# Performance work log

Hardware: AMD Instinct MI355X
Metric: run time of the kernel (lower is better)

The kernel has to match this reference:

```python
import jax, jax.numpy as jnp
import numpy as np

N_NODES = 50000
N_EDGES = 800000
HID = 128
N_PROC = 3  # num_layers - 1 processor iterations (shared weights)


def _mlp(x, w1, b1, w2, b2, w3, b3):
    h = jax.nn.relu(x @ w1 + b1)
    h = jax.nn.relu(h @ w2 + b2)
    return h @ w3 + b3


def setup_inputs() -> dict:
    key = jax.random.key(0)
    ks = jax.random.split(key, 32)

    def p(k, shape):
        fan_in = shape[0]
        return (jax.random.normal(k, shape, dtype=jnp.float32) / np.float32(np.sqrt(fan_in)))

    inp = {
        "X_curr": jax.random.normal(ks[0], (N_NODES, 6), dtype=jnp.float32),
        "y_prev": jax.random.normal(ks[1], (N_NODES,), dtype=jnp.float32),
        "edge": jax.random.randint(ks[2], (2, N_EDGES), 0, N_NODES, dtype=jnp.int32),
        "mode": 0,
        # EdgeModel net: Linear(9,H) ReLU Linear(H,H) ReLU Linear(H,3)
        "ew1": p(ks[3], (9, HID)), "eb1": jnp.zeros((HID,), jnp.float32),
        "ew2": p(ks[4], (HID, HID)), "eb2": jnp.zeros((HID,), jnp.float32),
        "ew3": p(ks[5], (HID, 3)), "eb3": jnp.zeros((3,), jnp.float32),
        # NodeModel net: Linear(5,H) ReLU Linear(H,H) ReLU Linear(H,1)
        "nw1": p(ks[6], (5, HID)), "nb1": jnp.zeros((HID,), jnp.float32),
        "nw2": p(ks[7], (HID, HID)), "nb2": jnp.zeros((HID,), jnp.float32),
        "nw3": p(ks[8], (HID, 1)), "nb3": jnp.zeros((1,), jnp.float32),
        # decoder: Linear(5,H) ReLU Linear(H,H) ReLU Linear(H,H) ReLU Linear(H,1)
        "dw1": p(ks[9], (5, HID)), "db1": jnp.zeros((HID,), jnp.float32),
        "dw2": p(ks[10], (HID, HID)), "db2": jnp.zeros((HID,), jnp.float32),
        "dw3": p(ks[11], (HID, HID)), "db3": jnp.zeros((HID,), jnp.float32),
        "dw4": p(ks[12], (HID, 1)), "db4": jnp.zeros((1,), jnp.float32),
    }
    return inp


def reference(X_curr, y_prev,
              ew1, eb1, ew2, eb2, ew3, eb3,
              nw1, nb1, nw2, nb2, nw3, nb3,
              dw1, db1, dw2, db2, dw3, db3, dw4, db4,
              edge, mode):
    n = X_curr.shape[0]
    src_idx, dst_idx = edge[0], edge[1]
    # x_in = cat(X_curr[:, [0,1,2,4]], y_prev)  -> [N, 5]
    x = jnp.concatenate([X_curr[:, jnp.array([0, 1, 2, 4])], y_prev[:, None]], axis=-1)

    # _compute_edge_attr: grad_r = (f_dest - f_src) * disp_r
    xs, xd = x[src_idx], x[dst_idx]
    disp = xd[:, :3] - xs[:, :3]
    edge_attr = (xd[:, 4] - xs[:, 4])[:, None] * disp  # [E, 3]

    # degree for scatter-mean (nodes with no incoming edges aggregate to 0)
    deg = jax.ops.segment_sum(jnp.ones((edge.shape[1],), x.dtype), dst_idx, num_segments=n)
    inv_deg = jnp.where(deg > 0, 1.0 / jnp.maximum(deg, 1.0), 0.0)

    for _ in range(N_PROC):
        # EdgeModel
        xs, xd = x[src_idx], x[dst_idx]
        disp = xd[:, :3] - xs[:, :3]
        norm_r = jnp.linalg.norm(disp, axis=-1, keepdims=True)
        net_in = jnp.concatenate([disp, norm_r, edge_attr, xs[:, 4:5], xd[:, 4:5]], axis=-1)  # [E, 9]
        edge_attr = edge_attr + _mlp(net_in, ew1, eb1, ew2, eb2, ew3, eb3)
        # NodeModel: message = edge_attr, aggr='mean' at target (edge[1])
        aggr = jax.ops.segment_sum(edge_attr, dst_idx, num_segments=n) * inv_deg[:, None]  # [N, 3]
        node_in = jnp.concatenate([x[:, 3:5], aggr], axis=-1)  # [N, 5]
        delta = _mlp(node_in, nw1, nb1, nw2, nb2, nw3, nb3)[:, 0]
        x = x.at[:, 4].add(delta)

    # decoder
    h = jax.nn.relu(x @ dw1 + db1)
    h = jax.nn.relu(h @ dw2 + db2)
    h = jax.nn.relu(h @ dw3 + db3)
    x_out = h @ dw4 + db4  # [N, 1]
    return y_prev + x_out[:, 0]
```

## Files before the change

kernel.cpp:

```cpp
#include <hip/hip_runtime.h>

typedef float f32x4 __attribute__((ext_vector_type(4)));
typedef __bf16 bf16x8 __attribute__((ext_vector_type(8)));
typedef __bf16 bf16x4 __attribute__((ext_vector_type(4)));

#define WB_W1E 0
#define WB_W2E 4096
#define WB_W3E 20480
#define WB_W1N 22528
#define WB_W2N 26624
#define WB_W3N 43008
#define WB_W1D 45056
#define WB_W2D 49152
#define WB_W3D 65536
#define WB_W4D 81920
#define WB_TOTAL 83968

#define BKT_SHIFT 6
#define BKT_SZ 64

__global__ void k_prep(const float* __restrict__ ew1, const float* __restrict__ eb1,
                       const float* __restrict__ ew2, const float* __restrict__ ew3,
                       const float* __restrict__ nw1, const float* __restrict__ nb1,
                       const float* __restrict__ nw2, const float* __restrict__ nw3,
                       const float* __restrict__ dw1, const float* __restrict__ db1,
                       const float* __restrict__ dw2, const float* __restrict__ dw3,
                       const float* __restrict__ dw4, __bf16* __restrict__ wb) {
  int gid = blockIdx.x * 256 + threadIdx.x;
  if (gid >= WB_TOTAL) return;
  const float* srcs[10] = {ew1, ew2, ew3, nw1, nw2, nw3, dw1, dw2, dw3, dw4};
  const float* brow[10] = {eb1, 0, 0, nb1, 0, 0, db1, 0, 0, 0};
  const int Ks[10] = {9, 128, 128, 5, 128, 128, 5, 128, 128, 128};
  const int Ns[10] = {128, 128, 3, 128, 128, 1, 128, 128, 128, 1};
  const int CTs[10] = {8, 8, 1, 8, 8, 1, 8, 8, 8, 1};
  const int cum[11] = {0, 4096, 20480, 22528, 26624, 43008, 45056, 49152, 65536, 81920, 83968};
  int seg = 0;
  while (gid >= cum[seg + 1]) seg++;
  int li = gid - cum[seg];
  int j = li & 7;
  int lane = (li >> 3) & 63;
  int fi = li >> 9;
  int CT = CTs[seg];
  int ct = fi % CT;
  int kt = fi / CT;
  int k = kt * 32 + ((lane >> 4) << 3) + j;
  int n = ct * 16 + (lane & 15);
  int kl;
  if (seg == 0) {
    if (k < 4) kl = k;
    else if (k >= 8 && k < 13) kl = k - 4;
    else kl = (k == 13) ? -2 : -1;
  } else if (seg == 3 || seg == 6) {
    if (k < 5) kl = k;
    else kl = (k == 5) ? -2 : -1;
  } else {
    kl = (k < Ks[seg]) ? k : -1;
  }
  float v = 0.f;
  if (n < Ns[seg]) {
    if (kl >= 0) v = srcs[seg][kl * Ns[seg] + n];
    else if (kl == -2 && brow[seg]) v = brow[seg][n];
  }
  wb[gid] = (__bf16)v;
}

__global__ void k_zero(const float* __restrict__ y_prev, float* __restrict__ x4,
                       int* __restrict__ cnt, int n) {
  int i = blockIdx.x * 256 + threadIdx.x;
  if (i < n) {
    x4[i] = y_prev[i];
    cnt[i] = 0;
  }
}

__global__ void k_count(const int* __restrict__ dstp, int* __restrict__ cnt, int E) {
  int e = blockIdx.x * 256 + threadIdx.x;
  if (e < E) atomicAdd(cnt + dstp[e], 1);
}

__global__ void k_scan_block(const int* __restrict__ cnt, int* __restrict__ rp,
                             float* __restrict__ invdeg, int* __restrict__ bsum, int n) {
  __shared__ int sd[256];
  int t = threadIdx.x;
  int i = blockIdx.x * 256 + t;
  int c = (i < n) ? cnt[i] : 0;
  if (i < n) invdeg[i] = c > 0 ? 1.0f / (float)c : 0.f;
  sd[t] = c;
  __syncthreads();
#pragma unroll
  for (int off = 1; off < 256; off <<= 1) {
    int v = sd[t];
    int u = (t >= off) ? sd[t - off] : 0;
    __syncthreads();
    sd[t] = v + u;
    __syncthreads();
  }
  if (i < n) rp[i] = sd[t] - c;
  if (t == 255) bsum[blockIdx.x] = sd[255];
}

__global__ void k_scan_top(int* __restrict__ bsum, int nb) {
  __shared__ int sd[1024];
  int t = threadIdx.x;
  int c = (t < nb) ? bsum[t] : 0;
  sd[t] = c;
  __syncthreads();
#pragma unroll
  for (int off = 1; off < 1024; off <<= 1) {
    int v = sd[t];
    int u = (t >= off) ? sd[t - off] : 0;
    __syncthreads();
    sd[t] = v + u;
    __syncthreads();
  }
  if (t < nb) bsum[t] = sd[t] - c;
}

__global__ void k_scan_add(int* __restrict__ rp, const int* __restrict__ bsum, int n, int E) {
  int i = blockIdx.x * 256 + threadIdx.x;
  if (i < n) rp[i] += bsum[blockIdx.x];
  if (i == 0) rp[n] = E;
}

__global__ void k_initcur(const int* __restrict__ rp, int* __restrict__ cur, int nbkt, int n) {
  int b = blockIdx.x * 256 + threadIdx.x;
  if (b < nbkt) {
    int d = b << BKT_SHIFT;
    if (d > n) d = n;
    cur[b] = rp[d];
  }
}

__global__ __launch_bounds__(256) void k_bin(const int* __restrict__ dstp, int* __restrict__ cur,
                                             int* __restrict__ eix, int nbkt, int E) {
  __shared__ int hist[1024];
  __shared__ int base[1024];
  int tid = threadIdx.x;
  for (int t = tid; t < nbkt; t += 256) hist[t] = 0;
  __syncthreads();
  int e0 = blockIdx.x * 8192;
  int b[32], lr[32];
#pragma unroll
  for (int j = 0; j < 32; j++) {
    int e = e0 + j * 256 + tid;
    if (e < E) {
      b[j] = dstp[e] >> BKT_SHIFT;
      lr[j] = atomicAdd(&hist[b[j]], 1);
    } else {
      b[j] = -1;
      lr[j] = 0;
    }
  }
  __syncthreads();
  for (int t = tid; t < nbkt; t += 256) {
    int c = hist[t];
    base[t] = c ? atomicAdd(&cur[t], c) : 0;
  }
  __syncthreads();
#pragma unroll
  for (int j = 0; j < 32; j++)
    if (b[j] >= 0) eix[base[b[j]] + lr[j]] = e0 + j * 256 + tid;
}

__global__ __launch_bounds__(256) void k_build(const int* __restrict__ srcO,
                                               const int* __restrict__ dstO,
                                               const float* __restrict__ Xc,
                                               const float* __restrict__ yp,
                                               const int* __restrict__ rp, const int* eix,
                                               int* __restrict__ srcS, int* dstS,
                                               float* __restrict__ peS, float* __restrict__ eaS,
                                               int n) {
  __shared__ int rpl[BKT_SZ + 1];
  __shared__ int cnt[BKT_SZ];
  int tid = threadIdx.x;
  int d0 = blockIdx.x << BKT_SHIFT;
  if (tid <= BKT_SZ) {
    int d = d0 + tid;
    if (d > n) d = n;
    rpl[tid] = rp[d];
  }
  if (tid < BKT_SZ) cnt[tid] = 0;
  __syncthreads();
  int dlim = n - d0;
  if (dlim > BKT_SZ) dlim = BKT_SZ;
  int gstart = rpl[0], gend = rpl[dlim];
  int ei[16];
#pragma unroll
  for (int k = 0; k < 16; k++) {
    int p = gstart + k * 256 + tid;
    ei[k] = (p < gend) ? eix[p] : -1;
  }
  __syncthreads();
#pragma unroll
  for (int k = 0; k < 16; k++) {
    int e = ei[k];
    if (e < 0) continue;
    int s = srcO[e], d = dstO[e];
    float dx = Xc[d * 6 + 0] - Xc[s * 6 + 0];
    float dy = Xc[d * 6 + 1] - Xc[s * 6 + 1];
    float dz = Xc[d * 6 + 2] - Xc[s * 6 + 2];
    float nr = sqrtf(dx * dx + dy * dy + dz * dz);
    float w = yp[d] - yp[s];
    int r = atomicAdd(&cnt[d - d0], 1);
    int q = rpl[d - d0] + r;
    srcS[q] = s;
    dstS[q] = d;
    f32x4 pv = {dx, dy, dz, nr};
    *(f32x4*)(peS + 4 * q) = pv;
    f32x4 av = {w * dx, w * dy, w * dz, 0.f};
    *(f32x4*)(eaS + 4 * q) = av;
  }
}

__global__ void k_gather(const float* __restrict__ eaS, const int* __restrict__ rp,
                         const float* __restrict__ invdeg, float* __restrict__ aggr, int n) {
  int i = blockIdx.x * 256 + threadIdx.x;
  if (i >= n) return;
  int s = rp[i];
  int e = rp[i + 1];
  f32x4 acc = {0.f, 0.f, 0.f, 0.f};
#pragma unroll 2
  for (int p = s; p < e; p++) {
    f32x4 v = *(const f32x4*)(eaS + 4 * p);
    acc[0] += v[0];
    acc[1] += v[1];
    acc[2] += v[2];
  }
  float iv = invdeg[i];
  f32x4 o = {acc[0] * iv, acc[1] * iv, acc[2] * iv, 0.f};
  *(f32x4*)(aggr + 4 * i) = o;
}

__device__ __forceinline__ int aoff(int row, int b) { return (row * 256 + b) ^ ((row & 7) << 4); }

__device__ __forceinline__ void wg_sync() {
  asm volatile("s_waitcnt lgkmcnt(0)" ::: "memory");
  __builtin_amdgcn_s_barrier();
}

__device__ __forceinline__ bf16x4 relu_pack(f32x4 a) {
  bf16x4 p;
#pragma unroll
  for (int r = 0; r < 4; r++) {
    float v = a[r];
    p[r] = (__bf16)(v > 0.f ? v : 0.f);
  }
  return p;
}

__global__ __attribute__((amdgpu_flat_work_group_size(256, 256), amdgpu_waves_per_eu(3, 4))) void
k_edge(const float* __restrict__ x4, const float* __restrict__ pe, float* __restrict__ ea,
       const int* __restrict__ src, const int* __restrict__ dstp,
       const __bf16* __restrict__ W1f, const __bf16* __restrict__ W2f,
       const __bf16* __restrict__ W3f, const float* __restrict__ b2,
       const float* __restrict__ b3, int ntiles, int E) {
  __shared__ char Ab[16384];
  __shared__ char Bb[16384];
  const int tid = threadIdx.x;
  const int l = tid & 63, w = tid >> 6;
  const int col = l & 15, krow = l >> 4;
  const int rl = w * 16 + (l >> 2), chunk = l & 3;

  bf16x8 w1r[2], w2r[4][2], w3r[4];
#pragma unroll
  for (int t = 0; t < 2; t++) w1r[t] = *(const bf16x8*)(W1f + ((2 * w + t) << 9) + l * 8);
#pragma unroll
  for (int kt = 0; kt < 4; kt++)
#pragma unroll
    for (int t = 0; t < 2; t++)
      w2r[kt][t] = *(const bf16x8*)(W2f + ((kt * 8 + 2 * w + t) << 9) + l * 8);
#pragma unroll
  for (int kt = 0; kt < 4; kt++) w3r[kt] = *(const bf16x8*)(W3f + (kt << 9) + l * 8);
  f32x4 b2c[2];
#pragma unroll
  for (int t = 0; t < 2; t++) b2c[t] = *(const f32x4*)(b2 + (2 * w + t) * 16 + krow * 4);
  f32x4 b3i = {0.f, 0.f, 0.f, 0.f};
  if (krow == 0) {
    b3i[0] = b3[0];
    b3i[1] = b3[1];
    b3i[2] = b3[2];
  }

  int tile = blockIdx.x;
  if (tile >= ntiles) return;

  int e0 = tile * 64 + rl;
  int ec = e0 < E ? e0 : E - 1;
  int cs = src[ec], cd = dstp[ec];
  f32x4 cld = {0.f, 0.f, 0.f, 0.f};
  if (chunk < 2) cld = *(const f32x4*)(((chunk == 1) ? ea : pe) + 4 * ec);
  float cxs = 0.f, cxd = 0.f;
  if (chunk == 1) {
    cxs = x4[cs];
    cxd = x4[cd];
  }

  for (;;) {
    bf16x8 v;
#pragma unroll
    for (int q = 0; q < 8; q++) v[q] = (__bf16)0.f;
    if (chunk == 0) {
      v[0] = (__bf16)cld[0];
      v[1] = (__bf16)cld[1];
      v[2] = (__bf16)cld[2];
      v[3] = (__bf16)cld[3];
    } else if (chunk == 1) {
      v[0] = (__bf16)cld[0];
      v[1] = (__bf16)cld[1];
      v[2] = (__bf16)cld[2];
      v[3] = (__bf16)cxs;
      v[4] = (__bf16)cxd;
      v[5] = (__bf16)1.0f;
    }
    *(bf16x8*)(Ab + aoff(rl, chunk * 16)) = v;

    int nt = tile + (int)gridDim.x;
    bool hn = nt < ntiles;
    int tc = hn ? nt : tile;
    int en = tc * 64 + rl;
    if (en >= E) en = E - 1;
    int ns = src[en], nd = dstp[en];

    wg_sync();

    f32x4 h[4][2];
#pragma unroll
    for (int c = 0; c < 4; c++)
#pragma unroll
      for (int t = 0; t < 2; t++) {
        f32x4 z = {0.f, 0.f, 0.f, 0.f};
        h[c][t] = z;
      }
    bf16x8 bb[4];
#pragma unroll
    for (int c = 0; c < 4; c++) bb[c] = *(const bf16x8*)(Ab + aoff(c * 16 + col, krow * 16));
#pragma unroll
    for (int c = 0; c < 4; c++)
#pragma unroll
      for (int t = 0; t < 2; t++)
        h[c][t] = __builtin_amdgcn_mfma_f32_16x16x32_bf16(w1r[t], bb[c], h[c][t], 0, 0, 0);
#pragma unroll
    for (int c = 0; c < 4; c++)
#pragma unroll
      for (int t = 0; t < 2; t++)
        *(bf16x4*)(Bb + aoff(c * 16 + col, (2 * w + t) * 32 + krow * 8)) = relu_pack(h[c][t]);

    wg_sync();

    f32x4 nld = {0.f, 0.f, 0.f, 0.f};
    if (chunk < 2) nld = *(const f32x4*)(((chunk == 1) ? ea : pe) + 4 * en);
    float nxs = 0.f, nxd = 0.f;
    if (chunk == 1) {
      nxs = x4[ns];
      nxd = x4[nd];
    }

#pragma unroll
    for (int c = 0; c < 4; c++)
#pragma unroll
      for (int t = 0; t < 2; t++) h[c][t] = b2c[t];
#pragma unroll
    for (int kt = 0; kt < 4; kt++) {
#pragma unroll
      for (int c = 0; c < 4; c++)
        bb[c] = *(const bf16x8*)(Bb + aoff(c * 16 + col, kt * 64 + krow * 16));
#pragma unroll
      for (int c = 0; c < 4; c++)
#pragma unroll
        for (int t = 0; t < 2; t++)
          h[c][t] = __builtin_amdgcn_mfma_f32_16x16x32_bf16(w2r[kt][t], bb[c], h[c][t], 0, 0, 0);
    }
#pragma unroll
    for (int c = 0; c < 4; c++)
#pragma unroll
      for (int t = 0; t < 2; t++)
        *(bf16x4*)(Ab + aoff(c * 16 + col, (2 * w + t) * 32 + krow * 8)) = relu_pack(h[c][t]);

    wg_sync();

    f32x4 o = b3i;
#pragma unroll
    for (int kt = 0; kt < 4; kt++) {
      bf16x8 bq = *(const bf16x8*)(Ab + aoff(w * 16 + col, kt * 64 + krow * 16));
      o = __builtin_amdgcn_mfma_f32_16x16x32_bf16(w3r[kt], bq, o, 0, 0, 0);
    }

    if (krow == 0) {
      int e3 = tile * 64 + w * 16 + col;
      if (e3 < E) {
        f32x4 oe = *(const f32x4*)(ea + 4 * e3);
        f32x4 nv;
        nv[0] = oe[0] + o[0];
        nv[1] = oe[1] + o[1];
        nv[2] = oe[2] + o[2];
        nv[3] = 0.f;
        *(f32x4*)(ea + 4 * e3) = nv;
      }
    }

    if (!hn) break;
    tile = nt;
    cld = nld;
    cxs = nxs;
    cxd = nxd;
  }
}

__global__ __attribute__((amdgpu_flat_work_group_size(256, 256), amdgpu_waves_per_eu(3, 4))) void
k_node(float* __restrict__ x4, const float* __restrict__ Xc, const float* __restrict__ aggr,
       const __bf16* __restrict__ W1f, const __bf16* __restrict__ W2f,
       const __bf16* __restrict__ W3f, const float* __restrict__ b2,
       const float* __restrict__ b3, int n) {
  __shared__ char Ab[16384];
  __shared__ char Bb[16384];
  const int tid = threadIdx.x;
  const int l = tid & 63, w = tid >> 6;
  const int col = l & 15, krow = l >> 4;
  const int rl = w * 16 + (l >> 2), chunk = l & 3;

  bf16x8 w1r[2], w2r[4][2], w3r[4];
#pragma unroll
  for (int t = 0; t < 2; t++) w1r[t] = *(const bf16x8*)(W1f + ((2 * w + t) << 9) + l * 8);
#pragma unroll
  for (int kt = 0; kt < 4; kt++)
#pragma unroll
    for (int t = 0; t < 2; t++)
      w2r[kt][t] = *(const bf16x8*)(W2f + ((kt * 8 + 2 * w + t) << 9) + l * 8);
#pragma unroll
  for (int kt = 0; kt < 4; kt++) w3r[kt] = *(const bf16x8*)(W3f + (kt << 9) + l * 8);
  f32x4 b2c[2];
#pragma unroll
  for (int t = 0; t < 2; t++) b2c[t] = *(const f32x4*)(b2 + (2 * w + t) * 16 + krow * 4);
  float b3s = b3[0];

  int tile = blockIdx.x;
  int i0 = tile * 64 + rl;
  bool vi = i0 < n;
  int i = vi ? i0 : (n - 1);

  bf16x8 v;
#pragma unroll
  for (int q = 0; q < 8; q++) v[q] = (__bf16)0.f;
  if (chunk == 0) {
    float x3 = Xc[i * 6 + 4];
    float xv = x4[i];
    f32x4 ag = *(const f32x4*)(aggr + 4 * i);
    v[0] = (__bf16)x3;
    v[1] = (__bf16)xv;
    v[2] = (__bf16)ag[0];
    v[3] = (__bf16)ag[1];
    v[4] = (__bf16)ag[2];
    v[5] = (__bf16)1.0f;
  }
  *(bf16x8*)(Ab + aoff(rl, chunk * 16)) = v;

  wg_sync();

  f32x4 h[4][2];
#pragma unroll
  for (int c = 0; c < 4; c++)
#pragma unroll
    for (int t = 0; t < 2; t++) {
      f32x4 z = {0.f, 0.f, 0.f, 0.f};
      h[c][t] = z;
    }
  bf16x8 bb[4];
#pragma unroll
  for (int c = 0; c < 4; c++) bb[c] = *(const bf16x8*)(Ab + aoff(c * 16 + col, krow * 16));
#pragma unroll
  for (int c = 0; c < 4; c++)
#pragma unroll
    for (int t = 0; t < 2; t++)
      h[c][t] = __builtin_amdgcn_mfma_f32_16x16x32_bf16(w1r[t], bb[c], h[c][t], 0, 0, 0);
#pragma unroll
  for (int c = 0; c < 4; c++)
#pragma unroll
    for (int t = 0; t < 2; t++)
      *(bf16x4*)(Bb + aoff(c * 16 + col, (2 * w + t) * 32 + krow * 8)) = relu_pack(h[c][t]);

  wg_sync();

#pragma unroll
  for (int c = 0; c < 4; c++)
#pragma unroll
    for (int t = 0; t < 2; t++) h[c][t] = b2c[t];
#pragma unroll
  for (int kt = 0; kt < 4; kt++) {
#pragma unroll
    for (int c = 0; c < 4; c++)
      bb[c] = *(const bf16x8*)(Bb + aoff(c * 16 + col, kt * 64 + krow * 16));
#pragma unroll
    for (int c = 0; c < 4; c++)
#pragma unroll
      for (int t = 0; t < 2; t++)
        h[c][t] = __builtin_amdgcn_mfma_f32_16x16x32_bf16(w2r[kt][t], bb[c], h[c][t], 0, 0, 0);
  }
#pragma unroll
  for (int c = 0; c < 4; c++)
#pragma unroll
    for (int t = 0; t < 2; t++)
      *(bf16x4*)(Ab + aoff(c * 16 + col, (2 * w + t) * 32 + krow * 8)) = relu_pack(h[c][t]);

  wg_sync();

  f32x4 o = {0.f, 0.f, 0.f, 0.f};
  if (krow == 0) o[0] = b3s;
#pragma unroll
  for (int kt = 0; kt < 4; kt++) {
    bf16x8 bq = *(const bf16x8*)(Ab + aoff(w * 16 + col, kt * 64 + krow * 16));
    o = __builtin_amdgcn_mfma_f32_16x16x32_bf16(w3r[kt], bq, o, 0, 0, 0);
  }

  if (krow == 0) {
    int i3 = tile * 64 + w * 16 + col;
    if (i3 < n) x4[i3] = x4[i3] + o[0];
  }
}

__global__ __attribute__((amdgpu_flat_work_group_size(256, 256), amdgpu_waves_per_eu(2, 4))) void
k_dec(const float* __restrict__ x4, const float* __restrict__ Xc, const float* __restrict__ y_prev,
      const __bf16* __restrict__ W1f, const __bf16* __restrict__ W2f,
      const __bf16* __restrict__ W3f, const __bf16* __restrict__ W4f,
      const float* __restrict__ b2, const float* __restrict__ b3, const float* __restrict__ b4,
      float* __restrict__ out, int n) {
  __shared__ char Ab[16384];
  __shared__ char Bb[16384];
  const int tid = threadIdx.x;
  const int l = tid & 63, w = tid >> 6;
  const int col = l & 15, krow = l >> 4;
  const int rl = w * 16 + (l >> 2), chunk = l & 3;

  bf16x8 w1r[2], w2r[4][2], w3r[4][2], w4r[4];
#pragma unroll
  for (int t = 0; t < 2; t++) w1r[t] = *(const bf16x8*)(W1f + ((2 * w + t) << 9) + l * 8);
#pragma unroll
  for (int kt = 0; kt < 4; kt++)
#pragma unroll
    for (int t = 0; t < 2; t++) {
      w2r[kt][t] = *(const bf16x8*)(W2f + ((kt * 8 + 2 * w + t) << 9) + l * 8);
      w3r[kt][t] = *(const bf16x8*)(W3f + ((kt * 8 + 2 * w + t) << 9) + l * 8);
    }
#pragma unroll
  for (int kt = 0; kt < 4; kt++) w4r[kt] = *(const bf16x8*)(W4f + (kt << 9) + l * 8);
  f32x4 b2c[2], b3c[2];
#pragma unroll
  for (int t = 0; t < 2; t++) {
    b2c[t] = *(const f32x4*)(b2 + (2 * w + t) * 16 + krow * 4);
    b3c[t] = *(const f32x4*)(b3 + (2 * w + t) * 16 + krow * 4);
  }
  float b4s = b4[0];

  int tile = blockIdx.x;
  int i0 = tile * 64 + rl;
  bool vi = i0 < n;
  int i = vi ? i0 : (n - 1);

  bf16x8 v;
#pragma unroll
  for (int q = 0; q < 8; q++) v[q] = (__bf16)0.f;
  if (chunk == 0) {
    v[0] = (__bf16)Xc[i * 6 + 0];
    v[1] = (__bf16)Xc[i * 6 + 1];
    v[2] = (__bf16)Xc[i * 6 + 2];
    v[3] = (__bf16)Xc[i * 6 + 4];
    v[4] = (__bf16)x4[i];
    v[5] = (__bf16)1.0f;
  }
  *(bf16x8*)(Ab + aoff(rl, chunk * 16)) = v;

  wg_sync();

  f32x4 h[4][2];
  bf16x8 bb[4];
#pragma unroll
  for (int c = 0; c < 4; c++)
#pragma unroll
    for (int t = 0; t < 2; t++) {
      f32x4 z = {0.f, 0.f, 0.f, 0.f};
      h[c][t] = z;
    }
#pragma unroll
  for (int c = 0; c < 4; c++) bb[c] = *(const bf16x8*)(Ab + aoff(c * 16 + col, krow * 16));
#pragma unroll
  for (int c = 0; c < 4; c++)
#pragma unroll
    for (int t = 0; t < 2; t++)
      h[c][t] = __builtin_amdgcn_mfma_f32_16x16x32_bf16(w1r[t], bb[c], h[c][t], 0, 0, 0);
#pragma unroll
  for (int c = 0; c < 4; c++)
#pragma unroll
    for (int t = 0; t < 2; t++)
      *(bf16x4*)(Bb + aoff(c * 16 + col, (2 * w + t) * 32 + krow * 8)) = relu_pack(h[c][t]);

  wg_sync();

#pragma unroll
  for (int c = 0; c < 4; c++)
#pragma unroll
    for (int t = 0; t < 2; t++) h[c][t] = b2c[t];
#pragma unroll
  for (int kt = 0; kt < 4; kt++) {
#pragma unroll
    for (int c = 0; c < 4; c++)
      bb[c] = *(const bf16x8*)(Bb + aoff(c * 16 + col, kt * 64 + krow * 16));
#pragma unroll
    for (int c = 0; c < 4; c++)
#pragma unroll
      for (int t = 0; t < 2; t++)
        h[c][t] = __builtin_amdgcn_mfma_f32_16x16x32_bf16(w2r[kt][t], bb[c], h[c][t], 0, 0, 0);
  }
#pragma unroll
  for (int c = 0; c < 4; c++)
#pragma unroll
    for (int t = 0; t < 2; t++)
      *(bf16x4*)(Ab + aoff(c * 16 + col, (2 * w + t) * 32 + krow * 8)) = relu_pack(h[c][t]);

  wg_sync();

#pragma unroll
  for (int c = 0; c < 4; c++)
#pragma unroll
    for (int t = 0; t < 2; t++) h[c][t] = b3c[t];
#pragma unroll
  for (int kt = 0; kt < 4; kt++) {
#pragma unroll
    for (int c = 0; c < 4; c++)
      bb[c] = *(const bf16x8*)(Ab + aoff(c * 16 + col, kt * 64 + krow * 16));
#pragma unroll
    for (int c = 0; c < 4; c++)
#pragma unroll
      for (int t = 0; t < 2; t++)
        h[c][t] = __builtin_amdgcn_mfma_f32_16x16x32_bf16(w3r[kt][t], bb[c], h[c][t], 0, 0, 0);
  }
#pragma unroll
  for (int c = 0; c < 4; c++)
#pragma unroll
    for (int t = 0; t < 2; t++)
      *(bf16x4*)(Bb + aoff(c * 16 + col, (2 * w + t) * 32 + krow * 8)) = relu_pack(h[c][t]);

  wg_sync();

  f32x4 o = {0.f, 0.f, 0.f, 0.f};
  if (krow == 0) o[0] = b4s;
#pragma unroll
  for (int kt = 0; kt < 4; kt++) {
    bf16x8 bq = *(const bf16x8*)(Bb + aoff(w * 16 + col, kt * 64 + krow * 16));
    o = __builtin_amdgcn_mfma_f32_16x16x32_bf16(w4r[kt], bq, o, 0, 0, 0);
  }

  if (krow == 0) {
    int i3 = tile * 64 + w * 16 + col;
    if (i3 < n) out[i3] = y_prev[i3] + o[0];
  }
}

extern "C" void kernel_launch(void* const* d_in, const int* in_sizes, int n_in, void* d_out,
                              int out_size, void* d_ws, size_t ws_size, hipStream_t stream) {
  const float* Xc = (const float*)d_in[0];
  const float* y_prev = (const float*)d_in[1];
  const int* edge = (const int*)d_in[2];
  const float* ew1 = (const float*)d_in[4];
  const float* eb1 = (const float*)d_in[5];
  const float* ew2 = (const float*)d_in[6];
  const float* eb2 = (const float*)d_in[7];
  const float* ew3 = (const float*)d_in[8];
  const float* eb3 = (const float*)d_in[9];
  const float* nw1 = (const float*)d_in[10];
  const float* nb1 = (const float*)d_in[11];
  const float* nw2 = (const float*)d_in[12];
  const float* nb2 = (const float*)d_in[13];
  const float* nw3 = (const float*)d_in[14];
  const float* nb3 = (const float*)d_in[15];
  const float* dw1 = (const float*)d_in[16];
  const float* db1 = (const float*)d_in[17];
  const float* dw2 = (const float*)d_in[18];
  const float* db2 = (const float*)d_in[19];
  const float* dw3 = (const float*)d_in[20];
  const float* db3 = (const float*)d_in[21];
  const float* dw4 = (const float*)d_in[22];
  const float* db4 = (const float*)d_in[23];

  int n = in_sizes[0] / 6;
  int E = in_sizes[2] / 2;
  const int* srcp = edge;
  const int* dstp = edge + E;

  __bf16* wb = (__bf16*)d_ws;
  float* fbase = (float*)((char*)d_ws + (size_t)WB_TOTAL * 2);
  size_t na = ((size_t)n + 3) & ~(size_t)3;
  float* x4 = fbase;
  float* invdeg = fbase + na;
  float* aggr = fbase + 2 * na;
  int* cnt = (int*)(fbase + 6 * na);
  int* rp = cnt + na;
  int* bsum = rp + na + 8;
  int* srcS = bsum + 1024;
  int* dstS = srcS + E;
  float* peS = (float*)(dstS + E);
  float* eaS = peS + 4 * (size_t)E;

  size_t need = (size_t)WB_TOTAL * 2 + (8 * na + 8 + 1024 + 10 * (size_t)E) * 4;
  if (ws_size < need) return;

  dim3 B(256);
  int nblk = (n + 255) / 256;
  int nbkt = (n + BKT_SZ - 1) / BKT_SZ;
  k_prep<<<dim3((WB_TOTAL + 255) / 256), B, 0, stream>>>(ew1, eb1, ew2, ew3, nw1, nb1, nw2, nw3,
                                                         dw1, db1, dw2, dw3, dw4, wb);
  k_zero<<<dim3(nblk), B, 0, stream>>>(y_prev, x4, cnt, n);
  k_count<<<dim3((E + 255) / 256), B, 0, stream>>>(dstp, cnt, E);
  k_scan_block<<<dim3(nblk), B, 0, stream>>>(cnt, rp, invdeg, bsum, n);
  k_scan_top<<<dim3(1), dim3(1024), 0, stream>>>(bsum, nblk);
  k_scan_add<<<dim3(nblk), B, 0, stream>>>(rp, bsum, n, E);
  k_initcur<<<dim3((nbkt + 255) / 256), B, 0, stream>>>(rp, bsum, nbkt, n);
  k_bin<<<dim3((E + 8191) / 8192), B, 0, stream>>>(dstp, bsum, dstS, nbkt, E);
  k_build<<<dim3(nbkt), B, 0, stream>>>(srcp, dstp, Xc, y_prev, rp, dstS, srcS, dstS, peS, eaS, n);

  int etiles = (E + 63) / 64;
  int vtiles = (n + 63) / 64;
  int egrid = etiles < 768 ? etiles : 768;
  for (int it = 0; it < 3; it++) {
    k_edge<<<dim3(egrid), B, 0, stream>>>(x4, peS, eaS, srcS, dstS, wb + WB_W1E, wb + WB_W2E,
                                          wb + WB_W3E, eb2, eb3, etiles, E);
    k_gather<<<dim3((n + 255) / 256), B, 0, stream>>>(eaS, rp, invdeg, aggr, n);
    k_node<<<dim3(vtiles), B, 0, stream>>>(x4, Xc, aggr, wb + WB_W1N, wb + WB_W2N, wb + WB_W3N,
                                           nb2, nb3, n);
  }
  k_dec<<<dim3(vtiles), B, 0, stream>>>(x4, Xc, y_prev, wb + WB_W1D, wb + WB_W2D, wb + WB_W3D,
                                        wb + WB_W4D, db2, db3, db4, (float*)d_out, n);
}
```

Baseline: 303.1 us.

## Fuse segment-mean gather into node kernel and fold cursor init into scan

Removes the separate k_gather kernel. Each node row's four lanes now sum its CSR-sorted edge attributes with a strided loop and shuffle reduction inside k_node, which drops the aggr buffer round-trip and one launch per iteration. The bucket cursor initialisation moves into k_scan_add, removing the k_initcur launch. The edge kernel's waves_per_eu hint is widened and its persistent grid cap raised from 768 to 2048 blocks, trading register budget for more resident waves.

```diff
diff --git a/kernel.cpp b/kernel.cpp
--- a/kernel.cpp
+++ b/kernel.cpp
@@ -116,19 +116,15 @@
   if (t < nb) bsum[t] = sd[t] - c;
 }
 
-__global__ void k_scan_add(int* __restrict__ rp, const int* __restrict__ bsum, int n, int E) {
+__global__ void k_scan_add(int* __restrict__ rp, const int* __restrict__ bsum,
+                           int* __restrict__ cur, int n, int E) {
   int i = blockIdx.x * 256 + threadIdx.x;
-  if (i < n) rp[i] += bsum[blockIdx.x];
+  if (i < n) {
+    int v = rp[i] + bsum[blockIdx.x];
+    rp[i] = v;
+    if ((i & (BKT_SZ - 1)) == 0) cur[i >> BKT_SHIFT] = v;
+  }
   if (i == 0) rp[n] = E;
-}
-
-__global__ void k_initcur(const int* __restrict__ rp, int* __restrict__ cur, int nbkt, int n) {
-  int b = blockIdx.x * 256 + threadIdx.x;
-  if (b < nbkt) {
-    int d = b << BKT_SHIFT;
-    if (d > n) d = n;
-    cur[b] = rp[d];
-  }
 }
 
 __global__ __launch_bounds__(256) void k_bin(const int* __restrict__ dstp, int* __restrict__ cur,
@@ -212,25 +208,6 @@
   }
 }
 
-__global__ void k_gather(const float* __restrict__ eaS, const int* __restrict__ rp,
-                         const float* __restrict__ invdeg, float* __restrict__ aggr, int n) {
-  int i = blockIdx.x * 256 + threadIdx.x;
-  if (i >= n) return;
-  int s = rp[i];
-  int e = rp[i + 1];
-  f32x4 acc = {0.f, 0.f, 0.f, 0.f};
-#pragma unroll 2
-  for (int p = s; p < e; p++) {
-    f32x4 v = *(const f32x4*)(eaS + 4 * p);
-    acc[0] += v[0];
-    acc[1] += v[1];
-    acc[2] += v[2];
-  }
-  float iv = invdeg[i];
-  f32x4 o = {acc[0] * iv, acc[1] * iv, acc[2] * iv, 0.f};
-  *(f32x4*)(aggr + 4 * i) = o;
-}
-
 __device__ __forceinline__ int aoff(int row, int b) { return (row * 256 + b) ^ ((row & 7) << 4); }
 
 __device__ __forceinline__ void wg_sync() {
@@ -248,7 +225,7 @@
   return p;
 }
 
-__global__ __attribute__((amdgpu_flat_work_group_size(256, 256), amdgpu_waves_per_eu(3, 4))) void
+__global__ __attribute__((amdgpu_flat_work_group_size(256, 256), amdgpu_waves_per_eu(2, 8))) void
 k_edge(const float* __restrict__ x4, const float* __restrict__ pe, float* __restrict__ ea,
        const int* __restrict__ src, const int* __restrict__ dstp,
        const __bf16* __restrict__ W1f, const __bf16* __restrict__ W2f,
@@ -407,7 +384,8 @@
 }
 
 __global__ __attribute__((amdgpu_flat_work_group_size(256, 256), amdgpu_waves_per_eu(3, 4))) void
-k_node(float* __restrict__ x4, const float* __restrict__ Xc, const float* __restrict__ aggr,
+k_node(float* __restrict__ x4, const float* __restrict__ Xc, const float* __restrict__ eaS,
+       const int* __restrict__ rp, const float* __restrict__ invdeg,
        const __bf16* __restrict__ W1f, const __bf16* __restrict__ W2f,
        const __bf16* __restrict__ W3f, const float* __restrict__ b2,
        const float* __restrict__ b3, int n) {
@@ -438,18 +416,33 @@
   bool vi = i0 < n;
   int i = vi ? i0 : (n - 1);
 
+  int ss = rp[i], se = rp[i + 1];
+  float a0 = 0.f, a1 = 0.f, a2 = 0.f;
+  for (int p = ss + chunk; p < se; p += 4) {
+    f32x4 ev = *(const f32x4*)(eaS + 4 * p);
+    a0 += ev[0];
+    a1 += ev[1];
+    a2 += ev[2];
+  }
+  a0 += __shfl_xor(a0, 1);
+  a1 += __shfl_xor(a1, 1);
+  a2 += __shfl_xor(a2, 1);
+  a0 += __shfl_xor(a0, 2);
+  a1 += __shfl_xor(a1, 2);
+  a2 += __shfl_xor(a2, 2);
+
   bf16x8 v;
 #pragma unroll
   for (int q = 0; q < 8; q++) v[q] = (__bf16)0.f;
   if (chunk == 0) {
     float x3 = Xc[i * 6 + 4];
     float xv = x4[i];
-    f32x4 ag = *(const f32x4*)(aggr + 4 * i);
+    float iv = invdeg[i];
     v[0] = (__bf16)x3;
     v[1] = (__bf16)xv;
-    v[2] = (__bf16)ag[0];
-    v[3] = (__bf16)ag[1];
-    v[4] = (__bf16)ag[2];
+    v[2] = (__bf16)(a0 * iv);
+    v[3] = (__bf16)(a1 * iv);
+    v[4] = (__bf16)(a2 * iv);
     v[5] = (__bf16)1.0f;
   }
   *(bf16x8*)(Ab + aoff(rl, chunk * 16)) = v;
@@ -690,16 +683,16 @@
   size_t na = ((size_t)n + 3) & ~(size_t)3;
   float* x4 = fbase;
   float* invdeg = fbase + na;
-  float* aggr = fbase + 2 * na;
-  int* cnt = (int*)(fbase + 6 * na);
+  int* cnt = (int*)(fbase + 2 * na);
   int* rp = cnt + na;
   int* bsum = rp + na + 8;
-  int* srcS = bsum + 1024;
+  int* cur = bsum + 1024;
+  int* srcS = cur + 1024;
   int* dstS = srcS + E;
   float* peS = (float*)(dstS + E);
   float* eaS = peS + 4 * (size_t)E;
 
-  size_t need = (size_t)WB_TOTAL * 2 + (8 * na + 8 + 1024 + 10 * (size_t)E) * 4;
+  size_t need = (size_t)WB_TOTAL * 2 + (4 * na + 8 + 2048 + 10 * (size_t)E) * 4;
   if (ws_size < need) return;
 
   dim3 B(256);
@@ -711,20 +704,18 @@
   k_count<<<dim3((E + 255) / 256), B, 0, stream>>>(dstp, cnt, E);
   k_scan_block<<<dim3(nblk), B, 0, stream>>>(cnt, rp, invdeg, bsum, n);
   k_scan_top<<<dim3(1), dim3(1024), 0, stream>>>(bsum, nblk);
-  k_scan_add<<<dim3(nblk), B, 0, stream>>>(rp, bsum, n, E);
-  k_initcur<<<dim3((nbkt + 255) / 256), B, 0, stream>>>(rp, bsum, nbkt, n);
-  k_bin<<<dim3((E + 8191) / 8192), B, 0, stream>>>(dstp, bsum, dstS, nbkt, E);
+  k_scan_add<<<dim3(nblk), B, 0, stream>>>(rp, bsum, cur, n, E);
+  k_bin<<<dim3((E + 8191) / 8192), B, 0, stream>>>(dstp, cur, dstS, nbkt, E);
   k_build<<<dim3(nbkt), B, 0, stream>>>(srcp, dstp, Xc, y_prev, rp, dstS, srcS, dstS, peS, eaS, n);
 
   int etiles = (E + 63) / 64;
   int vtiles = (n + 63) / 64;
-  int egrid = etiles < 768 ? etiles : 768;
+  int egrid = etiles < 2048 ? etiles : 2048;
   for (int it = 0; it < 3; it++) {
     k_edge<<<dim3(egrid), B, 0, stream>>>(x4, peS, eaS, srcS, dstS, wb + WB_W1E, wb + WB_W2E,
                                           wb + WB_W3E, eb2, eb3, etiles, E);
-    k_gather<<<dim3((n + 255) / 256), B, 0, stream>>>(eaS, rp, invdeg, aggr, n);
-    k_node<<<dim3(vtiles), B, 0, stream>>>(x4, Xc, aggr, wb + WB_W1N, wb + WB_W2N, wb + WB_W3N,
-                                           nb2, nb3, n);
+    k_node<<<dim3(vtiles), B, 0, stream>>>(x4, Xc, eaS, rp, invdeg, wb + WB_W1N, wb + WB_W2N,
+                                           wb + WB_W3N, nb2, nb3, n);
   }
   k_dec<<<dim3(vtiles), B, 0, stream>>>(x4, Xc, y_prev, wb + WB_W1D, wb + WB_W2D, wb + WB_W3D,
                                         wb + WB_W4D, db2, db3, db4, (float*)d_out, n);
```

New measurement: 296.8 us. -2.1%, faster.
